# Kernel tuning notes

Measured on AMD Instinct MI355X. Metric: run time of the kernel, lower is better.

Reference implementation:

```python
import jax, jax.numpy as jnp
import numpy as np

N_HEAD = 12
NEG = 1e9


def setup_inputs() -> dict:
    key = jax.random.key(0)
    k1, k2, k3 = jax.random.split(key, 3)
    B, S, D = 1, 4096, 768
    x = jax.random.normal(k1, (B, S, D), dtype=jnp.float32)
    w_attn = jax.random.normal(k2, (D, 3 * D), dtype=jnp.float32) * 0.02
    b_attn = jnp.zeros((3 * D,), dtype=jnp.float32)
    w_proj = jax.random.normal(k3, (D, D), dtype=jnp.float32) * 0.02
    b_proj = jnp.zeros((D,), dtype=jnp.float32)
    return {"x": x, "w_attn": w_attn, "b_attn": b_attn, "w_proj": w_proj, "b_proj": b_proj}


def reference(x, w_attn, b_attn, w_proj, b_proj):
    B, S, D = x.shape
    H = N_HEAD
    hd = D // H
    qkv = x @ w_attn + b_attn  # [B,S,3D]
    q, k, v = jnp.split(qkv, 3, axis=-1)
    # split heads -> [B,H,S,hd]
    q = q.reshape(B, S, H, hd).transpose(0, 2, 1, 3)
    k = k.reshape(B, S, H, hd).transpose(0, 2, 1, 3)
    v = v.reshape(B, S, H, hd).transpose(0, 2, 1, 3)
    w = jnp.einsum('bhqd,bhkd->bhqk', q, k) / jnp.sqrt(jnp.float32(hd))
    mask = jnp.tril(jnp.ones((S, S), dtype=w.dtype))  # causal tril buffer
    w = w * mask - NEG * (1.0 - mask)
    w = jax.nn.softmax(w, axis=-1)
    a = jnp.einsum('bhqk,bhkd->bhqd', w, v)
    a = a.transpose(0, 2, 1, 3).reshape(B, S, D)  # merge heads
    return a @ w_proj + b_proj
```

## Files before the change

### kernel.cpp

```cpp
#include <hip/hip_runtime.h>

typedef __bf16 bf16x8 __attribute__((ext_vector_type(8)));
typedef float f32x4 __attribute__((ext_vector_type(4)));
typedef float f32x16 __attribute__((ext_vector_type(16)));
typedef unsigned short u16;

__device__ inline u16 f2bf(float f) {
  union { float f; unsigned int u; } v; v.f = f;
  unsigned int r = v.u + 0x7fffu + ((v.u >> 16) & 1u);
  return (u16)(r >> 16);
}

__device__ inline void load_lds16(const void* g, void* l) {
  __builtin_amdgcn_global_load_lds((const __attribute__((address_space(1))) unsigned int*)g,
                                   (__attribute__((address_space(3))) unsigned int*)l, 16, 0, 0);
}

__global__ void cvt_bf16(const float* __restrict__ in, u16* __restrict__ out, int n) {
  int i = (blockIdx.x * blockDim.x + threadIdx.x) * 4;
  if (i < n) {
    float4 v = *(const float4*)(in + i);
    ushort4 o;
    o.x = f2bf(v.x); o.y = f2bf(v.y); o.z = f2bf(v.z); o.w = f2bf(v.w);
    *(ushort4*)(out + i) = o;
  }
}

__global__ void transpose_cvt(const float* __restrict__ in, u16* __restrict__ out, int R, int C) {
  __shared__ float tile[32][33];
  int c0 = blockIdx.x * 32, r0 = blockIdx.y * 32;
  int tx = threadIdx.x;
#pragma unroll
  for (int i = threadIdx.y; i < 32; i += 8)
    tile[i][tx] = in[(size_t)(r0 + i) * C + c0 + tx];
  __syncthreads();
#pragma unroll
  for (int i = threadIdx.y; i < 32; i += 8)
    out[(size_t)(c0 + i) * R + r0 + tx] = f2bf(tile[tx][i]);
}

__global__ __launch_bounds__(256) void vtrans(const u16* __restrict__ qkv, u16* __restrict__ vT) {
  const int h = blockIdx.y;
  const int s0 = blockIdx.x * 64;
  const int tid = threadIdx.x;
  __shared__ u16 T[64][72];
  {
    const int key = tid >> 2, dq = (tid & 3) * 16;
    const u16* g = qkv + (size_t)(s0 + key) * 2304 + 1536 + h * 64 + dq;
    *(uint4*)&T[key][dq] = *(const uint4*)g;
    *(uint4*)&T[key][dq + 8] = *(const uint4*)(g + 8);
  }
  __syncthreads();
  {
    const int d = tid >> 2, sq = (tid & 3) * 16;
    u16 tmp[16];
#pragma unroll
    for (int e = 0; e < 16; ++e) tmp[e] = T[sq + e][d];
    u16* o = vT + ((size_t)h * 64 + d) * 4096 + s0 + sq;
    *(uint4*)o = *(uint4*)tmp;
    *(uint4*)(o + 8) = *(uint4*)(tmp + 8);
  }
}

template <int BF16_OUT>
__global__ __launch_bounds__(256) void gemm_bt(const u16* __restrict__ A, const u16* __restrict__ BT,
                                               const float* __restrict__ bias, void* __restrict__ Cv,
                                               int M, int N, int K) {
  __shared__ __align__(16) u16 As[128 * 32];
  __shared__ __align__(16) u16 Bs[128 * 32];
  const int tid = threadIdx.x;
  const int wave = tid >> 6, lane = tid & 63;
  const int g = lane >> 4, lr = lane & 15;
  const int m0 = blockIdx.y * 128, n0 = blockIdx.x * 128;
  const int wr = (wave >> 1) * 64, wc = (wave & 1) * 64;
  f32x4 acc[4][4] = {};

  for (int k0 = 0; k0 < K; k0 += 32) {
    __syncthreads();
#pragma unroll
    for (int j = 0; j < 2; ++j) {
      const int e = tid * 8 + j * 2048;
      const int r = e >> 5, c = e & 31;
      const u16* ga = A + (size_t)(m0 + r) * K + k0 + c;
      const u16* gb = BT + (size_t)(n0 + r) * K + k0 + c;
      load_lds16(ga, (void*)(As + wave * 512 + j * 2048));
      load_lds16(gb, (void*)(Bs + wave * 512 + j * 2048));
    }
    __syncthreads();
    const u16* pa = As + (wr + lr) * 32 + g * 8;
    const u16* pb = Bs + (wc + lr) * 32 + g * 8;
    bf16x8 a[4], b[4];
#pragma unroll
    for (int i = 0; i < 4; ++i) a[i] = *(const bf16x8*)(pa + i * 16 * 32);
#pragma unroll
    for (int j = 0; j < 4; ++j) b[j] = *(const bf16x8*)(pb + j * 16 * 32);
#pragma unroll
    for (int i = 0; i < 4; ++i)
#pragma unroll
      for (int j = 0; j < 4; ++j)
        acc[i][j] = __builtin_amdgcn_mfma_f32_16x16x32_bf16(a[i], b[j], acc[i][j], 0, 0, 0);
  }

#pragma unroll
  for (int i = 0; i < 4; ++i)
#pragma unroll
    for (int j = 0; j < 4; ++j)
#pragma unroll
      for (int r = 0; r < 4; ++r) {
        int row = m0 + wr + i * 16 + g * 4 + r;
        int col = n0 + wc + j * 16 + lr;
        float v = acc[i][j][r] + bias[col];
        if (BF16_OUT)
          ((u16*)Cv)[(size_t)row * N + col] = f2bf(v);
        else
          ((float*)Cv)[(size_t)row * N + col] = v;
      }
}

#define MNEG 30000.0f
template <int CH, int DIRECT>
__global__ __launch_bounds__(256, 3) void attn(const u16* __restrict__ qkv, const u16* __restrict__ vT,
                                               u16* __restrict__ pO, float* __restrict__ pml,
                                               u16* __restrict__ aout) {
  __shared__ __align__(16) u16 KV[4][4096];

  const int bid = blockIdx.x;
  const int h = bid % 12;
  int g, c;
  if (DIRECT) {
    g = 31 - bid / 12;
    c = 0;
  } else {
    const int u = 79 - bid / 12;
    if (u < 8) { g = u; c = 0; }
    else if (u < 24) { g = 8 + ((u - 8) >> 1); c = (u - 8) & 1; }
    else if (u < 48) { g = 16 + (u - 24) / 3; c = (u - 24) % 3; }
    else { g = 24 + ((u - 48) >> 2); c = (u - 48) & 3; }
  }

  const int tid = threadIdx.x;
  const int wave = tid >> 6;
  const int l = tid & 63;
  const int lr = l & 31;
  const int H = l >> 5;
  const int H4 = H * 4, H8 = H * 8;

  const int qt = 4 * g + wave;
  const int q0 = qt * 32;
  const int nkt = (qt >> 1) + 1;
  const int t0 = DIRECT ? 0 : c * CH;
  const int tend = min(2 * g + 2, t0 + CH);

  const u16* kgb = qkv + 768 + h * 64;
  const u16* vgb = vT + (size_t)h * 64 * 4096;

  const int srow = l >> 3;
  int kSo[2], vSo[2];
#pragma unroll
  for (int i = 0; i < 2; ++i) {
    const int row = 16 * wave + 8 * i + srow;
    const int sc = ((l & 7) ^ srow ^ (2 * wave + i)) << 3;
    kSo[i] = row * 2304 + sc;
    vSo[i] = row * 4096 + sc;
  }

  const u16* Rd[2][4];
#pragma unroll
  for (int b2 = 0; b2 < 2; ++b2) {
    const int row = 32 * b2 + lr;
    const int sw = (row ^ (row >> 3)) & 7;
#pragma unroll
    for (int cc = 0; cc < 4; ++cc)
      Rd[b2][cc] = &KV[0][row * 64 + (((2 * cc + H) ^ sw) << 3)];
  }

  bf16x8 qB[4];
  {
    const u16* qp = qkv + (size_t)(q0 + lr) * 2304 + h * 64;
    const float qs = 0.125f * 1.4426950408889634f;
#pragma unroll
    for (int cc = 0; cc < 4; ++cc) {
      bf16x8 raw = *(const bf16x8*)(qp + 16 * cc + H8);
#pragma unroll
      for (int e = 0; e < 8; ++e) qB[cc][e] = (__bf16)((float)raw[e] * qs);
    }
  }

  f32x16 O[2] = {};
  float mst = -MNEG, lst = 0.f;

#define STAGE(T, BUF)                                                      \
  {                                                                        \
    const size_t kk = (size_t)(T) * 64;                                    \
    _Pragma("unroll") for (int i = 0; i < 2; ++i) {                        \
      load_lds16(kgb + kk * 2304 + kSo[i], &KV[(BUF)][(2 * wave + i) * 512]); \
      load_lds16(vgb + kk + vSo[i], &KV[2 + (BUF)][(2 * wave + i) * 512]); \
    }                                                                      \
  }

#define BODY(T, BUF)                                                                        \
  {                                                                                         \
    if ((T) + 1 < tend) {                                                                   \
      STAGE((T) + 1, (BUF) ^ 1);                                                            \
      asm volatile("s_waitcnt vmcnt(4)" ::: "memory");                                      \
    } else {                                                                                \
      asm volatile("s_waitcnt vmcnt(0)" ::: "memory");                                      \
    }                                                                                       \
    __builtin_amdgcn_s_barrier();                                                           \
    __builtin_amdgcn_sched_barrier(0);                                                      \
    f32x16 s[2] = {};                                                                       \
    _Pragma("unroll") for (int kb = 0; kb < 2; ++kb)                                        \
      _Pragma("unroll") for (int cc = 0; cc < 4; ++cc) {                                    \
        bf16x8 kf = *(const bf16x8*)(Rd[kb][cc] + (BUF) * 4096);                            \
        s[kb] = __builtin_amdgcn_mfma_f32_32x32x16_bf16(kf, qB[cc], s[kb], 0, 0, 0);        \
      }                                                                                     \
    bf16x8 vf[2][4];                                                                        \
    _Pragma("unroll") for (int da = 0; da < 2; ++da)                                        \
      _Pragma("unroll") for (int cc = 0; cc < 4; ++cc)                                      \
        vf[da][cc] = *(const bf16x8*)(Rd[da][cc] + 8192 + (BUF) * 4096);                    \
    if ((T) >= nkt - 1) {                                                                   \
      const int rel = q0 + lr - (T) * 64;                                                   \
      _Pragma("unroll") for (int kb = 0; kb < 2; ++kb)                                      \
        _Pragma("unroll") for (int r = 0; r < 16; ++r)                                      \
          if (32 * kb + (r & 3) + 8 * (r >> 2) + H4 > rel) s[kb][r] = -MNEG;                \
    }                                                                                       \
    float mx = s[0][0];                                                                     \
    _Pragma("unroll") for (int kb = 0; kb < 2; ++kb)                                        \
      _Pragma("unroll") for (int r = 0; r < 16; ++r) mx = fmaxf(mx, s[kb][r]);              \
    mx = fmaxf(mx, __shfl_xor(mx, 32));                                                     \
    if (__any(mx > mst + 12.f)) {                                                           \
      const float mn = fmaxf(mst, mx);                                                      \
      const float alpha = __builtin_amdgcn_exp2f(mst - mn);                                 \
      mst = mn;                                                                             \
      lst *= alpha;                                                                         \
      O[0] *= alpha;                                                                        \
      O[1] *= alpha;                                                                        \
    }                                                                                       \
    float rs = 0.f;                                                                         \
    _Pragma("unroll") for (int kb = 0; kb < 2; ++kb)                                        \
      _Pragma("unroll") for (int r = 0; r < 16; ++r) {                                      \
        const float p = __builtin_amdgcn_exp2f(s[kb][r] - mst);                             \
        s[kb][r] = p;                                                                       \
        rs += p;                                                                            \
      }                                                                                     \
    rs += __shfl_xor(rs, 32);                                                               \
    lst += rs;                                                                              \
    unsigned w[16];                                                                         \
    _Pragma("unroll") for (int kb = 0; kb < 2; ++kb)                                        \
      _Pragma("unroll") for (int j2 = 0; j2 < 4; ++j2) {                                    \
        asm("v_cvt_pk_bf16_f32 %0, %1, %2"                                                  \
            : "=v"(w[kb * 8 + j2 * 2]) : "v"(s[kb][4 * j2]), "v"(s[kb][4 * j2 + 1]));       \
        asm("v_cvt_pk_bf16_f32 %0, %1, %2"                                                  \
            : "=v"(w[kb * 8 + j2 * 2 + 1]) : "v"(s[kb][4 * j2 + 2]), "v"(s[kb][4 * j2 + 3])); \
      }                                                                                     \
    unsigned recv[8];                                                                       \
    _Pragma("unroll") for (int cc = 0; cc < 4; ++cc)                                        \
      _Pragma("unroll") for (int m = 0; m < 2; ++m) {                                       \
        const unsigned send = H ? w[4 * cc + m] : w[4 * cc + 2 + m];                        \
        recv[cc * 2 + m] = (unsigned)__shfl_xor((int)send, 32);                             \
      }                                                                                     \
    _Pragma("unroll") for (int cc = 0; cc < 4; ++cc) {                                      \
      union { unsigned u[4]; bf16x8 v; } Bp;                                                \
      Bp.u[0] = H ? recv[2 * cc] : w[4 * cc];                                               \
      Bp.u[1] = H ? recv[2 * cc + 1] : w[4 * cc + 1];                                       \
      Bp.u[2] = H ? w[4 * cc + 2] : recv[2 * cc];                                           \
      Bp.u[3] = H ? w[4 * cc + 3] : recv[2 * cc + 1];                                       \
      O[0] = __builtin_amdgcn_mfma_f32_32x32x16_bf16(vf[0][cc], Bp.v, O[0], 0, 0, 0);       \
      O[1] = __builtin_amdgcn_mfma_f32_32x32x16_bf16(vf[1][cc], Bp.v, O[1], 0, 0, 0);       \
    }                                                                                       \
    __builtin_amdgcn_s_barrier();                                                           \
  }

  STAGE(t0, 0);
  int t = t0;
  for (; t + 2 <= tend; t += 2) {
    BODY(t, 0);
    BODY(t + 1, 1);
  }
  if (t < tend) BODY(t, 0);
#undef BODY
#undef STAGE

  if (DIRECT) {
    const float inv = 1.0f / lst;
    u16* orow = aout + (size_t)(q0 + lr) * 768 + h * 64;
#pragma unroll
    for (int da = 0; da < 2; ++da)
#pragma unroll
      for (int j2 = 0; j2 < 4; ++j2) {
        ushort4 st;
        st.x = f2bf(O[da][4 * j2 + 0] * inv);
        st.y = f2bf(O[da][4 * j2 + 1] * inv);
        st.z = f2bf(O[da][4 * j2 + 2] * inv);
        st.w = f2bf(O[da][4 * j2 + 3] * inv);
        *(ushort4*)(orow + 32 * da + 8 * j2 + H4) = st;
      }
  } else {
    const int slot = (h * 128 + qt) * 4 + c;
    u16* po = pO + (size_t)slot * 2048 + lr * 64;
#pragma unroll
    for (int da = 0; da < 2; ++da)
#pragma unroll
      for (int j2 = 0; j2 < 4; ++j2) {
        ushort4 st;
        st.x = f2bf(O[da][4 * j2 + 0]);
        st.y = f2bf(O[da][4 * j2 + 1]);
        st.z = f2bf(O[da][4 * j2 + 2]);
        st.w = f2bf(O[da][4 * j2 + 3]);
        *(ushort4*)(po + 32 * da + 8 * j2 + H4) = st;
      }
    if (H == 0) {
      float2 ml; ml.x = mst; ml.y = lst;
      *(float2*)(pml + (size_t)slot * 64 + lr * 2) = ml;
    }
  }
}

__global__ __launch_bounds__(64) void combine(const u16* __restrict__ pO, const float* __restrict__ pml,
                                              u16* __restrict__ aout, int CHv) {
  const int bid = blockIdx.x;
  const int h = bid % 12, qt = bid / 12;
  const int nkt = (qt >> 1) + 1;
  const int nc = (nkt + CHv - 1) / CHv;
  const int sb = (h * 128 + qt) * 4;
  const int t = threadIdx.x;
  const int row = t & 31, H = t >> 5;

  float m[4], lw[4];
  float M = -__builtin_inff();
#pragma unroll
  for (int c = 0; c < 4; ++c)
    if (c < nc) {
      m[c] = pml[(size_t)(sb + c) * 64 + row * 2];
      M = fmaxf(M, m[c]);
    }
  float L = 0.f;
#pragma unroll
  for (int c = 0; c < 4; ++c)
    if (c < nc) {
      lw[c] = __builtin_amdgcn_exp2f(m[c] - M);
      L += pml[(size_t)(sb + c) * 64 + row * 2 + 1] * lw[c];
    }

  float acc[32] = {};
#pragma unroll
  for (int c = 0; c < 4; ++c)
    if (c < nc) {
      const u16* p = pO + (size_t)(sb + c) * 2048 + row * 64 + 32 * H;
      const float wgt = lw[c];
#pragma unroll
      for (int k = 0; k < 4; ++k) {
        bf16x8 v = *(const bf16x8*)(p + 8 * k);
#pragma unroll
        for (int e = 0; e < 8; ++e) acc[k * 8 + e] += (float)v[e] * wgt;
      }
    }

  const float inv = 1.0f / L;
  u16 ov[32];
#pragma unroll
  for (int d = 0; d < 32; ++d) ov[d] = f2bf(acc[d] * inv);
  u16* dst = aout + (size_t)(qt * 32 + row) * 768 + h * 64 + 32 * H;
#pragma unroll
  for (int k = 0; k < 4; ++k) *(uint4*)(dst + 8 * k) = *(const uint4*)(ov + 8 * k);
}

extern "C" void kernel_launch(void* const* d_in, const int* in_sizes, int n_in,
                              void* d_out, int out_size, void* d_ws, size_t ws_size,
                              hipStream_t stream) {
  const float* x = (const float*)d_in[0];
  const float* w_attn = (const float*)d_in[1];
  const float* b_attn = (const float*)d_in[2];
  const float* w_proj = (const float*)d_in[3];
  const float* b_proj = (const float*)d_in[4];
  float* out = (float*)d_out;

  const int S = 4096, D = 768;
  u16* xb = (u16*)d_ws;
  u16* wTa = xb + (size_t)S * D;
  u16* wTp = wTa + (size_t)3 * D * D;
  u16* qkv = wTp + (size_t)D * D;
  u16* abuf = qkv + (size_t)S * 3 * D;
  u16* vTb = abuf + (size_t)S * D;
  u16* pO = vTb + (size_t)12 * 64 * 4096;

  const size_t base_bytes = (size_t)(3145728 + 1769472 + 589824 + 9437184 + 3145728 + 3145728) * 2;
  const size_t need16 = base_bytes + (size_t)6144 * 2048 * 2 + (size_t)6144 * 64 * 4;

  cvt_bf16<<<(S * D) / 1024, 256, 0, stream>>>(x, xb, S * D);
  transpose_cvt<<<dim3((3 * D) / 32, D / 32), dim3(32, 8), 0, stream>>>(w_attn, wTa, D, 3 * D);
  transpose_cvt<<<dim3(D / 32, D / 32), dim3(32, 8), 0, stream>>>(w_proj, wTp, D, D);
  gemm_bt<1><<<dim3((3 * D) / 128, S / 128), 256, 0, stream>>>(xb, wTa, b_attn, qkv, S, 3 * D, D);
  vtrans<<<dim3(S / 64, 12), 256, 0, stream>>>(qkv, vTb);

  if (ws_size >= need16) {
    float* pml = (float*)(pO + (size_t)6144 * 2048);
    attn<16, 0><<<dim3(12 * 80), 256, 0, stream>>>(qkv, vTb, pO, pml, abuf);
    combine<<<dim3(12 * 128), 64, 0, stream>>>(pO, pml, abuf, 16);
  } else {
    attn<64, 1><<<dim3(12 * 32), 256, 0, stream>>>(qkv, vTb, abuf, (float*)abuf, abuf);
  }

  gemm_bt<0><<<dim3(D / 128, S / 128), 256, 0, stream>>>(abuf, wTp, b_proj, out, S, D, D);
}
```

Baseline: 143.4 us.

## Widen attention blocks to 8 waves sharing K/V tiles and add MFMA priority

Attention blocks grow from 4 to 8 waves (256 query rows per block), so each staged 64-key K/V tile in LDS serves twice as many query tiles. Each thread now issues half as many async loads per stage. The grid schedule and split-K chunking are remapped for the larger groups. s_setprio is raised around the MFMA sections to favour matrix work. The larger blocks may hurt occupancy and load balance across causal chunks.

```diff
diff --git a/kernel.cpp b/kernel.cpp
--- a/kernel.cpp
+++ b/kernel.cpp
@@ -118,24 +118,24 @@
 }
 
 #define MNEG 30000.0f
-template <int CH, int DIRECT>
-__global__ __launch_bounds__(256, 3) void attn(const u16* __restrict__ qkv, const u16* __restrict__ vT,
+template <int DIRECT>
+__global__ __launch_bounds__(512, 4) void attn(const u16* __restrict__ qkv, const u16* __restrict__ vT,
                                                u16* __restrict__ pO, float* __restrict__ pml,
                                                u16* __restrict__ aout) {
   __shared__ __align__(16) u16 KV[4][4096];
 
   const int bid = blockIdx.x;
   const int h = bid % 12;
-  int g, c;
+  int gp, c;
   if (DIRECT) {
-    g = 31 - bid / 12;
+    gp = 15 - bid / 12;
     c = 0;
   } else {
-    const int u = 79 - bid / 12;
-    if (u < 8) { g = u; c = 0; }
-    else if (u < 24) { g = 8 + ((u - 8) >> 1); c = (u - 8) & 1; }
-    else if (u < 48) { g = 16 + (u - 24) / 3; c = (u - 24) % 3; }
-    else { g = 24 + ((u - 48) >> 2); c = (u - 48) & 3; }
+    const int u = bid / 12;
+    if (u < 16) { gp = 15 - (u >> 2); c = u & 3; }
+    else if (u < 28) { gp = 11 - (u - 16) / 3; c = (u - 16) % 3; }
+    else if (u < 36) { gp = 7 - ((u - 28) >> 1); c = (u - 28) & 1; }
+    else { gp = 3 - (u - 36); c = 0; }
   }
 
   const int tid = threadIdx.x;
@@ -145,24 +145,19 @@
   const int H = l >> 5;
   const int H4 = H * 4, H8 = H * 8;
 
-  const int qt = 4 * g + wave;
+  const int qt = 8 * gp + wave;
   const int q0 = qt * 32;
   const int nkt = (qt >> 1) + 1;
-  const int t0 = DIRECT ? 0 : c * CH;
-  const int tend = min(2 * g + 2, t0 + CH);
+  const int t0 = DIRECT ? 0 : c * 16;
+  const int tend = min(4 * gp + 4, t0 + 16);
 
   const u16* kgb = qkv + 768 + h * 64;
   const u16* vgb = vT + (size_t)h * 64 * 4096;
 
   const int srow = l >> 3;
-  int kSo[2], vSo[2];
-#pragma unroll
-  for (int i = 0; i < 2; ++i) {
-    const int row = 16 * wave + 8 * i + srow;
-    const int sc = ((l & 7) ^ srow ^ (2 * wave + i)) << 3;
-    kSo[i] = row * 2304 + sc;
-    vSo[i] = row * 4096 + sc;
-  }
+  const int sc = ((l & 7) ^ srow ^ wave) << 3;
+  const int kSo = (8 * wave + srow) * 2304 + sc;
+  const int vSo = (8 * wave + srow) * 4096 + sc;
 
   const u16* Rd[2][4];
 #pragma unroll
@@ -189,31 +184,31 @@
   f32x16 O[2] = {};
   float mst = -MNEG, lst = 0.f;
 
-#define STAGE(T, BUF)                                                      \
-  {                                                                        \
-    const size_t kk = (size_t)(T) * 64;                                    \
-    _Pragma("unroll") for (int i = 0; i < 2; ++i) {                        \
-      load_lds16(kgb + kk * 2304 + kSo[i], &KV[(BUF)][(2 * wave + i) * 512]); \
-      load_lds16(vgb + kk + vSo[i], &KV[2 + (BUF)][(2 * wave + i) * 512]); \
-    }                                                                      \
+#define STAGE(T, BUF)                                                   \
+  {                                                                     \
+    const size_t kk = (size_t)(T) * 64;                                 \
+    load_lds16(kgb + kk * 2304 + kSo, &KV[(BUF)][wave * 512]);          \
+    load_lds16(vgb + kk + vSo, &KV[2 + (BUF)][wave * 512]);             \
   }
 
 #define BODY(T, BUF)                                                                        \
   {                                                                                         \
     if ((T) + 1 < tend) {                                                                   \
       STAGE((T) + 1, (BUF) ^ 1);                                                            \
-      asm volatile("s_waitcnt vmcnt(4)" ::: "memory");                                      \
+      asm volatile("s_waitcnt vmcnt(2)" ::: "memory");                                      \
     } else {                                                                                \
       asm volatile("s_waitcnt vmcnt(0)" ::: "memory");                                      \
     }                                                                                       \
     __builtin_amdgcn_s_barrier();                                                           \
     __builtin_amdgcn_sched_barrier(0);                                                      \
     f32x16 s[2] = {};                                                                       \
+    __builtin_amdgcn_s_setprio(1);                                                          \
     _Pragma("unroll") for (int kb = 0; kb < 2; ++kb)                                        \
       _Pragma("unroll") for (int cc = 0; cc < 4; ++cc) {                                    \
         bf16x8 kf = *(const bf16x8*)(Rd[kb][cc] + (BUF) * 4096);                            \
         s[kb] = __builtin_amdgcn_mfma_f32_32x32x16_bf16(kf, qB[cc], s[kb], 0, 0, 0);        \
       }                                                                                     \
+    __builtin_amdgcn_s_setprio(0);                                                          \
     bf16x8 vf[2][4];                                                                        \
     _Pragma("unroll") for (int da = 0; da < 2; ++da)                                        \
       _Pragma("unroll") for (int cc = 0; cc < 4; ++cc)                                      \
@@ -259,6 +254,7 @@
         const unsigned send = H ? w[4 * cc + m] : w[4 * cc + 2 + m];                        \
         recv[cc * 2 + m] = (unsigned)__shfl_xor((int)send, 32);                             \
       }                                                                                     \
+    __builtin_amdgcn_s_setprio(1);                                                          \
     _Pragma("unroll") for (int cc = 0; cc < 4; ++cc) {                                      \
       union { unsigned u[4]; bf16x8 v; } Bp;                                                \
       Bp.u[0] = H ? recv[2 * cc] : w[4 * cc];                                               \
@@ -268,6 +264,7 @@
       O[0] = __builtin_amdgcn_mfma_f32_32x32x16_bf16(vf[0][cc], Bp.v, O[0], 0, 0, 0);       \
       O[1] = __builtin_amdgcn_mfma_f32_32x32x16_bf16(vf[1][cc], Bp.v, O[1], 0, 0, 0);       \
     }                                                                                       \
+    __builtin_amdgcn_s_setprio(0);                                                          \
     __builtin_amdgcn_s_barrier();                                                           \
   }
 
@@ -395,10 +392,10 @@
 
   if (ws_size >= need16) {
     float* pml = (float*)(pO + (size_t)6144 * 2048);
-    attn<16, 0><<<dim3(12 * 80), 256, 0, stream>>>(qkv, vTb, pO, pml, abuf);
+    attn<0><<<dim3(12 * 40), 512, 0, stream>>>(qkv, vTb, pO, pml, abuf);
     combine<<<dim3(12 * 128), 64, 0, stream>>>(pO, pml, abuf, 16);
   } else {
-    attn<64, 1><<<dim3(12 * 32), 256, 0, stream>>>(qkv, vTb, abuf, (float*)abuf, abuf);
+    attn<1><<<dim3(12 * 16), 512, 0, stream>>>(qkv, vTb, abuf, (float*)abuf, abuf);
   }
 
   gemm_bt<0><<<dim3(D / 128, S / 128), 256, 0, stream>>>(abuf, wTp, b_proj, out, S, D, D);
```

Result: slower. 226.8 us (+58.2%).
